# Performance work log

Hardware: AMD Instinct MI355X
Metric: run time of the kernel (lower is better)

Reference implementation:

```python
import jax, jax.numpy as jnp
import numpy as np

S, N, IN_F, OUT_F = 8, 200000, 128, 128

def setup_inputs() -> dict:
    key = jax.random.key(0)
    k1, k2, k3, k4 = jax.random.split(key, 4)
    support_matmul_input = jax.random.normal(k1, (S, N, IN_F), dtype=jnp.float32)
    weight = jax.random.normal(k2, (S, IN_F, OUT_F), dtype=jnp.float32)
    layer_attention = jax.random.normal(k3, (S,), dtype=jnp.float32)
    bias = jax.random.normal(k4, (OUT_F,), dtype=jnp.float32)
    return {
        "support_matmul_input": support_matmul_input,
        "weight": weight,
        "layer_attention": layer_attention,
        "bias": bias,
    }

def reference(support_matmul_input, weight, layer_attention, bias):
    # Faithful math: out[n,o] = sum_s attn[s] * (X[s] @ W[s])[n,o] + bias[o]
    # Expressed as a single fused einsum over the support dim; equivalent to
    # torch's matmul -> permute -> mul(attn) -> sum(dim=2) -> +bias.
    out = jnp.einsum("sni,sio,s->no", support_matmul_input, weight, layer_attention)
    return out + bias
```

## Files before the change

kernel.cpp:

```cpp
#include <hip/hip_runtime.h>


typedef __bf16 bf16x8 __attribute__((ext_vector_type(8)));
typedef float  f32x4  __attribute__((ext_vector_type(4)));

#define N_DIM 200000
#define LDSS  72

__global__ void prep_w_kernel(const float* __restrict__ W,
                              const float* __restrict__ attn,
                              __bf16* __restrict__ Wt) {
    const int idx = blockIdx.x * 256 + threadIdx.x;
    const int o = idx >> 10;
    const int k = idx & 1023;
    const int s = k >> 7;
    const float v = attn[s] * W[(size_t)k * 128 + o];
    Wt[((size_t)(k >> 6) * 128 + o) * 64 + (k & 63)] = (__bf16)v;
}

__global__ __launch_bounds__(256, 2)
void mgc_kernel(const float* __restrict__ X,
                const __bf16* __restrict__ Wt,
                const float* __restrict__ bias,
                float* __restrict__ out) {
    __shared__ __bf16 As[128 * LDSS];
    __shared__ __bf16 Bs[128 * LDSS];

    const int tid  = threadIdx.x;
    const int lane = tid & 63;
    const int wave = tid >> 6;
    const int wr   = (wave >> 1) * 64;
    const int wc   = (wave & 1) * 64;
    const int l15  = lane & 15;
    const int quad = lane >> 4;

    const long n0 = (long)blockIdx.x * 128;

    f32x4 acc[4][4] = {};

    const int ara = tid >> 3;
    const int ack = (tid & 7) * 8;

    #pragma unroll 1
    for (int kb = 0; kb < 16; ++kb) {
        const int s  = kb >> 1;
        const int i0 = (kb & 1) * 64;
        const float*  Ablk = X  + ((size_t)s * N_DIM + (size_t)n0) * 128 + i0;
        const __bf16* Bblk = Wt + (size_t)kb * 8192;

        __syncthreads();

        #pragma unroll
        for (int p = 0; p < 4; ++p) {
            const int r = ara + p * 32;
            f32x4 v0 = {0.f, 0.f, 0.f, 0.f}, v1 = {0.f, 0.f, 0.f, 0.f};
            if (n0 + r < N_DIM) {
                const f32x4* src = (const f32x4*)(Ablk + (size_t)r * 128 + ack);
                v0 = src[0];
                v1 = src[1];
            }
            bf16x8 w;
            w[0] = (__bf16)v0.x; w[1] = (__bf16)v0.y; w[2] = (__bf16)v0.z; w[3] = (__bf16)v0.w;
            w[4] = (__bf16)v1.x; w[5] = (__bf16)v1.y; w[6] = (__bf16)v1.z; w[7] = (__bf16)v1.w;
            *(bf16x8*)(&As[r * LDSS + ack]) = w;
        }

        #pragma unroll
        for (int j = 0; j < 4; ++j) {
            const int e = (j * 256 + tid) * 8;
            bf16x8 v = *(const bf16x8*)(Bblk + e);
            *(bf16x8*)(&Bs[(e >> 6) * LDSS + (e & 63)]) = v;
        }

        __syncthreads();

        #pragma unroll
        for (int kk = 0; kk < 64; kk += 32) {
            bf16x8 af[4], bfr[4];
            #pragma unroll
            for (int t = 0; t < 4; ++t)
                af[t] = *(const bf16x8*)(&As[(wr + t * 16 + l15) * LDSS + kk + quad * 8]);
            #pragma unroll
            for (int t = 0; t < 4; ++t)
                bfr[t] = *(const bf16x8*)(&Bs[(wc + t * 16 + l15) * LDSS + kk + quad * 8]);
            #pragma unroll
            for (int i = 0; i < 4; ++i)
                #pragma unroll
                for (int j = 0; j < 4; ++j)
                    acc[i][j] = __builtin_amdgcn_mfma_f32_16x16x32_bf16(af[i], bfr[j], acc[i][j], 0, 0, 0);
        }
    }

    float bv[4];
    #pragma unroll
    for (int j = 0; j < 4; ++j)
        bv[j] = bias[wc + j * 16 + l15];

    #pragma unroll
    for (int i = 0; i < 4; ++i) {
        #pragma unroll
        for (int reg = 0; reg < 4; ++reg) {
            const long r = n0 + wr + i * 16 + quad * 4 + reg;
            if (r < N_DIM) {
                float* orow = out + r * 128 + wc + l15;
                #pragma unroll
                for (int j = 0; j < 4; ++j)
                    orow[j * 16] = acc[i][j][reg] + bv[j];
            }
        }
    }
}

extern "C" void kernel_launch(void* const* d_in, const int* in_sizes, int n_in,
                              void* d_out, int out_size, void* d_ws, size_t ws_size,
                              hipStream_t stream) {
    const float* X    = (const float*)d_in[0];
    const float* W    = (const float*)d_in[1];
    const float* attn = (const float*)d_in[2];
    const float* bias = (const float*)d_in[3];
    float* out = (float*)d_out;
    __bf16* Wt = (__bf16*)d_ws;

    prep_w_kernel<<<512, 256, 0, stream>>>(W, attn, Wt);
    const int nblocks = (N_DIM + 127) / 128;
    mgc_kernel<<<nblocks, 256, 0, stream>>>(X, Wt, bias, out);
}
```

Before: 1.081 ms.

## Drop LDS staging; load X and W fragments directly into registers per wave

Removes the shared-memory tiles and block barriers. Each wave now owns 32 rows and all 128 output columns, loading X fragments from global memory straight into MFMA register layout and reading the bf16 W tile directly from global/L2. Output stores become nontemporal. This trades LDS traffic and syncs for less coalesced global loads (16-lane row-strided fp32 reads) and redundant W reads per wave. N_DIM is a multiple of 32, so dropping the bounds checks does not break correctness.

New measurement: 1.221 ms. 1.13x slower.

```diff
diff --git a/kernel.cpp b/kernel.cpp
--- a/kernel.cpp
+++ b/kernel.cpp
@@ -5,7 +5,6 @@
 typedef float  f32x4  __attribute__((ext_vector_type(4)));
 
 #define N_DIM 200000
-#define LDSS  72
 
 __global__ void prep_w_kernel(const float* __restrict__ W,
                               const float* __restrict__ attn,
@@ -23,90 +22,81 @@
                 const __bf16* __restrict__ Wt,
                 const float* __restrict__ bias,
                 float* __restrict__ out) {
-    __shared__ __bf16 As[128 * LDSS];
-    __shared__ __bf16 Bs[128 * LDSS];
-
     const int tid  = threadIdx.x;
     const int lane = tid & 63;
     const int wave = tid >> 6;
-    const int wr   = (wave >> 1) * 64;
-    const int wc   = (wave & 1) * 64;
     const int l15  = lane & 15;
     const int quad = lane >> 4;
 
     const long n0 = (long)blockIdx.x * 128;
+    const long r0 = n0 + wave * 32;
+    if (r0 >= N_DIM) return;
 
-    f32x4 acc[4][4] = {};
-
-    const int ara = tid >> 3;
-    const int ack = (tid & 7) * 8;
+    f32x4 acc[2][8] = {};
 
     #pragma unroll 1
     for (int kb = 0; kb < 16; ++kb) {
         const int s  = kb >> 1;
         const int i0 = (kb & 1) * 64;
-        const float*  Ablk = X  + ((size_t)s * N_DIM + (size_t)n0) * 128 + i0;
-        const __bf16* Bblk = Wt + (size_t)kb * 8192;
+        const float*  Ab = X + ((size_t)s * N_DIM + (size_t)(r0 + l15)) * 128
+                             + i0 + quad * 8;
+        const __bf16* Bb = Wt + (size_t)kb * 8192 + (size_t)l15 * 64 + quad * 8;
 
-        __syncthreads();
+        f32x4 a[2][2][2];
+        #pragma unroll
+        for (int i = 0; i < 2; ++i)
+            #pragma unroll
+            for (int kx = 0; kx < 2; ++kx) {
+                const f32x4* p = (const f32x4*)(Ab + (size_t)(i * 16) * 128 + kx * 32);
+                a[i][kx][0] = p[0];
+                a[i][kx][1] = p[1];
+            }
+
+        bf16x8 bf[8][2];
+        #pragma unroll
+        for (int j = 0; j < 8; ++j)
+            #pragma unroll
+            for (int kx = 0; kx < 2; ++kx)
+                bf[j][kx] = *(const bf16x8*)(Bb + (size_t)j * 1024 + kx * 32);
+
+        bf16x8 abf[2][2];
+        #pragma unroll
+        for (int i = 0; i < 2; ++i)
+            #pragma unroll
+            for (int kx = 0; kx < 2; ++kx) {
+                const f32x4 v0 = a[i][kx][0], v1 = a[i][kx][1];
+                bf16x8 w;
+                w[0] = (__bf16)v0.x; w[1] = (__bf16)v0.y;
+                w[2] = (__bf16)v0.z; w[3] = (__bf16)v0.w;
+                w[4] = (__bf16)v1.x; w[5] = (__bf16)v1.y;
+                w[6] = (__bf16)v1.z; w[7] = (__bf16)v1.w;
+                abf[i][kx] = w;
+            }
 
         #pragma unroll
-        for (int p = 0; p < 4; ++p) {
-            const int r = ara + p * 32;
-            f32x4 v0 = {0.f, 0.f, 0.f, 0.f}, v1 = {0.f, 0.f, 0.f, 0.f};
-            if (n0 + r < N_DIM) {
-                const f32x4* src = (const f32x4*)(Ablk + (size_t)r * 128 + ack);
-                v0 = src[0];
-                v1 = src[1];
-            }
-            bf16x8 w;
-            w[0] = (__bf16)v0.x; w[1] = (__bf16)v0.y; w[2] = (__bf16)v0.z; w[3] = (__bf16)v0.w;
-            w[4] = (__bf16)v1.x; w[5] = (__bf16)v1.y; w[6] = (__bf16)v1.z; w[7] = (__bf16)v1.w;
-            *(bf16x8*)(&As[r * LDSS + ack]) = w;
-        }
-
-        #pragma unroll
-        for (int j = 0; j < 4; ++j) {
-            const int e = (j * 256 + tid) * 8;
-            bf16x8 v = *(const bf16x8*)(Bblk + e);
-            *(bf16x8*)(&Bs[(e >> 6) * LDSS + (e & 63)]) = v;
-        }
-
-        __syncthreads();
-
-        #pragma unroll
-        for (int kk = 0; kk < 64; kk += 32) {
-            bf16x8 af[4], bfr[4];
+        for (int kx = 0; kx < 2; ++kx)
             #pragma unroll
-            for (int t = 0; t < 4; ++t)
-                af[t] = *(const bf16x8*)(&As[(wr + t * 16 + l15) * LDSS + kk + quad * 8]);
-            #pragma unroll
-            for (int t = 0; t < 4; ++t)
-                bfr[t] = *(const bf16x8*)(&Bs[(wc + t * 16 + l15) * LDSS + kk + quad * 8]);
-            #pragma unroll
-            for (int i = 0; i < 4; ++i)
+            for (int i = 0; i < 2; ++i)
                 #pragma unroll
-                for (int j = 0; j < 4; ++j)
-                    acc[i][j] = __builtin_amdgcn_mfma_f32_16x16x32_bf16(af[i], bfr[j], acc[i][j], 0, 0, 0);
-        }
+                for (int j = 0; j < 8; ++j)
+                    acc[i][j] = __builtin_amdgcn_mfma_f32_16x16x32_bf16(
+                        abf[i][kx], bf[j][kx], acc[i][j], 0, 0, 0);
     }
 
-    float bv[4];
+    float bv[8];
     #pragma unroll
-    for (int j = 0; j < 4; ++j)
-        bv[j] = bias[wc + j * 16 + l15];
+    for (int j = 0; j < 8; ++j)
+        bv[j] = bias[j * 16 + l15];
 
     #pragma unroll
-    for (int i = 0; i < 4; ++i) {
+    for (int i = 0; i < 2; ++i) {
         #pragma unroll
         for (int reg = 0; reg < 4; ++reg) {
-            const long r = n0 + wr + i * 16 + quad * 4 + reg;
-            if (r < N_DIM) {
-                float* orow = out + r * 128 + wc + l15;
-                #pragma unroll
-                for (int j = 0; j < 4; ++j)
-                    orow[j * 16] = acc[i][j][reg] + bv[j];
-            }
+            const long r = r0 + i * 16 + quad * 4 + reg;
+            float* orow = out + r * 128 + l15;
+            #pragma unroll
+            for (int j = 0; j < 8; ++j)
+                __builtin_nontemporal_store(acc[i][j][reg] + bv[j], &orow[j * 16]);
         }
     }
 }
```
